# Performance work log

Hardware: AMD Instinct MI355X
Metric: run time of the kernel (lower is better)

Reference implementation:

```python
import jax, jax.numpy as jnp
import numpy as np
import math

# Model dims (see shape_source)
BATCH, SEQ, HH, WW = 32, 128, 32, 32   # x: (B, seq_len, H, W); L = H*W = 1024
D_MODEL = 1024                          # hidden_dim
N2 = 4                                  # n=8 -> 4 complex S4D modes
L_MAX = 64                              # SSM kernel length (l_max)


def _layernorm(x, gamma, beta, eps=1e-5):
    mu = jnp.mean(x, axis=-1, keepdims=True)
    var = jnp.var(x, axis=-1, keepdims=True)
    return (x - mu) * jax.lax.rsqrt(var + eps) * gamma + beta


def setup_inputs() -> dict:
    key = jax.random.key(0)
    ks = jax.random.split(key, 12)
    d_in = SEQ  # d_input = d_output = seq_len
    inp = {
        "x": jax.random.normal(ks[0], (BATCH, SEQ, HH, WW), dtype=jnp.float32),
        # encoder Linear(d_input -> d_model)
        "W_enc": jax.random.normal(ks[1], (d_in, D_MODEL), dtype=jnp.float32) / math.sqrt(d_in),
        "b_enc": jnp.zeros((D_MODEL,), dtype=jnp.float32),
        # S4D SSM parameters (per d_model channel, N2 complex modes)
        "log_dt": (jax.random.uniform(ks[2], (D_MODEL,), dtype=jnp.float32)
                   * (math.log(0.1) - math.log(0.001)) + math.log(0.001)),
        "A_log_real": jnp.full((D_MODEL, N2), math.log(0.5), dtype=jnp.float32),
        "A_imag": jnp.broadcast_to(math.pi * jnp.arange(N2, dtype=jnp.float32), (D_MODEL, N2)).copy(),
        "C_real": jax.random.normal(ks[3], (D_MODEL, N2), dtype=jnp.float32) * 0.5,
        "C_imag": jax.random.normal(ks[4], (D_MODEL, N2), dtype=jnp.float32) * 0.5,
        "D": jax.random.normal(ks[5], (D_MODEL,), dtype=jnp.float32),
        # position-wise GLU mixing Linear(d_model -> 2*d_model)
        "W_glu": jax.random.normal(ks[6], (D_MODEL, 2 * D_MODEL), dtype=jnp.float32) / math.sqrt(D_MODEL),
        "b_glu": jnp.zeros((2 * D_MODEL,), dtype=jnp.float32),
        "ln_gamma": jnp.ones((D_MODEL,), dtype=jnp.float32),
        "ln_beta": jnp.zeros((D_MODEL,), dtype=jnp.float32),
        # decoder Linear(d_model -> d_output)
        "W_dec": jax.random.normal(ks[7], (D_MODEL, d_in), dtype=jnp.float32) / math.sqrt(D_MODEL),
        "b_dec": jnp.zeros((d_in,), dtype=jnp.float32),
    }
    return inp


def reference(x, W_enc, b_enc, log_dt, A_log_real, A_imag, C_real, C_imag, D,
              W_glu, b_glu, ln_gamma, ln_beta, W_dec, b_dec):
    Bsz, S, Hh, Ww = x.shape
    L = Hh * Ww
    u = x.reshape(Bsz, S, L)                                  # (B, d_input, L)
    # encoder applied per position along L
    h = jnp.einsum('bdl,de->ble', u, W_enc) + b_enc           # (B, L, d_model)

    # ---- S4D kernel (ZOH discretization, B=1, diagonal A) ----
    dt = jnp.exp(log_dt)                                      # (d,)
    A = -jnp.exp(A_log_real) + 1j * A_imag                    # (d, n2) complex
    Cc = C_real + 1j * C_imag
    dtA = A * dt[:, None]                                     # (d, n2)
    Bd = (jnp.exp(dtA) - 1.0) / A                             # ZOH input matrix
    t = jnp.arange(L_MAX)
    vand = jnp.exp(dtA[:, :, None] * t)                       # (d, n2, l_max)
    K = 2.0 * jnp.einsum('dn,dnl->dl', Cc * Bd, vand).real    # (d, l_max)

    # ---- causal FFT convolution along L + skip D*u ----
    z = jnp.swapaxes(h, 1, 2)                                 # (B, d, L)
    n_fft = L + L_MAX
    y = jnp.fft.irfft(jnp.fft.rfft(z, n=n_fft) * jnp.fft.rfft(K, n=n_fft), n=n_fft)[..., :L]
    y = y + D[:, None] * z                                    # (B, d, L)

    # ---- block: GELU -> GLU mixing -> residual -> LayerNorm ----
    y = jax.nn.gelu(jnp.swapaxes(y, 1, 2))                    # (B, L, d)
    g = y @ W_glu + b_glu                                     # (B, L, 2d)
    g = g[..., :D_MODEL] * jax.nn.sigmoid(g[..., D_MODEL:])
    h = _layernorm(h + g, ln_gamma, ln_beta)                  # (B, L, d)

    out = h @ W_dec + b_dec                                   # (B, L, d_output)
    out = jnp.swapaxes(out, 1, 2).reshape(Bsz, S, Hh, Ww)
    return out
```

## Files before the change

### kernel.cpp

```cpp
#include <hip/hip_runtime.h>
#include <hip/hip_bf16.h>
#include <math.h>

#define B_ 32
#define S_ 128
#define L_ 1024
#define D_ 1024

typedef unsigned short u16;
typedef __attribute__((ext_vector_type(8))) __bf16 bf16x8;
typedef __attribute__((ext_vector_type(4))) float f32x4;

__device__ __forceinline__ float bf2f(u16 u) {
    return __uint_as_float(((unsigned)u) << 16);
}
__device__ __forceinline__ u16 f2bf(float f) {
    unsigned u = __float_as_uint(f);
    u += 0x7FFF + ((u >> 16) & 1);
    return (u16)(u >> 16);
}
__device__ __forceinline__ float gelu_tanh(float x) {
    float x3 = x * x * x;
    float t = tanhf(0.7978845608028654f * (x + 0.044715f * x3));
    return 0.5f * x * (1.0f + t);
}
__device__ __forceinline__ float sigmoidf(float x) {
    return 1.0f / (1.0f + expf(-x));
}
__device__ __forceinline__ void gld16(const void* g, void* l) {
    __builtin_amdgcn_global_load_lds((const __attribute__((address_space(1))) void*)g,
                                     (__attribute__((address_space(3))) void*)l, 16, 0, 0);
}

__global__ __launch_bounds__(256) void k_ssmk(
        const float* __restrict__ log_dt, const float* __restrict__ Alr,
        const float* __restrict__ Aim, const float* __restrict__ Cr,
        const float* __restrict__ Ci, float* __restrict__ Kt) {
    int tid = blockIdx.x * 256 + threadIdx.x;
    int d = tid & (D_ - 1);
    int j = tid >> 10;
    float dt = expf(log_dt[d]);
    float acc = 0.f;
    #pragma unroll
    for (int n = 0; n < 4; ++n) {
        float ar = -expf(Alr[d * 4 + n]);
        float ai = Aim[d * 4 + n];
        float wr = ar * dt, wi = ai * dt;
        float ew = expf(wr);
        float sw, cw; sincosf(wi, &sw, &cw);
        float ur = ew * cw - 1.0f, ui = ew * sw;
        float inv = 1.0f / (ar * ar + ai * ai);
        float bdr = (ur * ar + ui * ai) * inv;
        float bdi = (ui * ar - ur * ai) * inv;
        float cr = Cr[d * 4 + n], ci = Ci[d * 4 + n];
        float cbr = cr * bdr - ci * bdi;
        float cbi = cr * bdi + ci * bdr;
        float ej = expf(wr * (float)j);
        float sj, cj; sincosf(wi * (float)j, &sj, &cj);
        acc += 2.0f * ej * (cbr * cj - cbi * sj);
    }
    Kt[j * D_ + d] = acc;
}

__global__ __launch_bounds__(256) void k_zero(float* __restrict__ p) {
    int tid = blockIdx.x * 256 + threadIdx.x;
    *(float4*)&p[tid * 4] = make_float4(0.f, 0.f, 0.f, 0.f);
}

__global__ __launch_bounds__(256) void k_c12(
        const float* __restrict__ Wd, const float* __restrict__ gam,
        const float* __restrict__ bet, const float* __restrict__ bd,
        float* __restrict__ c12) {
    int s = blockIdx.x;
    int t = threadIdx.x;
    float a1 = 0.f, a2 = 0.f;
    #pragma unroll
    for (int it = 0; it < 4; ++it) {
        int k = it * 256 + t;
        float w = Wd[(size_t)k * 128 + s];
        a1 += gam[k] * w;
        a2 += bet[k] * w;
    }
    #pragma unroll
    for (int off = 32; off > 0; off >>= 1) {
        a1 += __shfl_down(a1, off);
        a2 += __shfl_down(a2, off);
    }
    __shared__ float r1[4], r2[4];
    int wid = t >> 6, lane = t & 63;
    if (lane == 0) { r1[wid] = a1; r2[wid] = a2; }
    __syncthreads();
    if (t == 0) {
        c12[s] = r1[0] + r1[1] + r1[2] + r1[3];
        c12[128 + s] = r2[0] + r2[1] + r2[2] + r2[3] + bd[s];
    }
}

__global__ __launch_bounds__(256) void k_tcast(
        const float* __restrict__ src0, u16* __restrict__ dst0, int R, int C,
        const float* __restrict__ rowscale) {
    __shared__ float tile[64][65];
    const float* src = src0 + (size_t)blockIdx.z * R * C;
    u16* dst = dst0 + (size_t)blockIdx.z * R * C;
    int c0 = blockIdx.x * 64;
    int r0 = blockIdx.y * 64;
    int t = threadIdx.x;
    #pragma unroll
    for (int p = 0; p < 4; ++p) {
        int fid = p * 256 + t;
        int rr = fid >> 4, cc = (fid & 15) * 4;
        float4 v = *(const float4*)&src[(size_t)(r0 + rr) * C + c0 + cc];
        float sc = rowscale ? rowscale[r0 + rr] : 1.0f;
        tile[rr][cc + 0] = v.x * sc; tile[rr][cc + 1] = v.y * sc;
        tile[rr][cc + 2] = v.z * sc; tile[rr][cc + 3] = v.w * sc;
    }
    __syncthreads();
    #pragma unroll
    for (int p = 0; p < 4; ++p) {
        int fid = p * 256 + t;
        int rr = fid >> 4, cc = (fid & 15) * 4;
        ushort4 o;
        o.x = f2bf(tile[cc + 0][rr]);
        o.y = f2bf(tile[cc + 1][rr]);
        o.z = f2bf(tile[cc + 2][rr]);
        o.w = f2bf(tile[cc + 3][rr]);
        *(ushort4*)&dst[(size_t)(c0 + rr) * R + r0 + cc] = o;
    }
}

__global__ __launch_bounds__(256) void k_enc_mfma(
        const u16* __restrict__ xb, const u16* __restrict__ WeT,
        const float* __restrict__ be, u16* __restrict__ hb) {
    __shared__ u16 As[128 * 128];
    __shared__ u16 Bs[128 * 128];
    int t = threadIdx.x;
    int lane = t & 63, wid = t >> 6;
    int wr = wid & 1, wc = wid >> 1;
    int orig = blockIdx.x;
    int wgid = (orig & 7) * 256 + (orig >> 3);
    int m0 = (wgid >> 3) * 128;
    int e0 = (wgid & 7) * 128;

    #pragma unroll
    for (int c = 0; c < 8; ++c) {
        int ch = wid * 8 + c;
        int r = ch * 4 + (lane >> 4);
        int g = (lane & 15) ^ (r & 15);
        gld16(&xb[(size_t)(m0 + r) * 128 + g * 8], &As[ch * 512]);
        gld16(&WeT[(size_t)(e0 + r) * 128 + g * 8], &Bs[ch * 512]);
    }
    int co4[4];
    #pragma unroll
    for (int kh = 0; kh < 4; ++kh)
        co4[kh] = ((((lane >> 4) + kh * 4) ^ (lane & 15)) * 8);
    int arow[4], brow[4];
    #pragma unroll
    for (int i = 0; i < 4; ++i) arow[i] = (wr * 64 + i * 16 + (lane & 15)) * 128;
    #pragma unroll
    for (int q = 0; q < 4; ++q) brow[q] = (wc * 64 + q * 16 + (lane & 15)) * 128;

    __syncthreads();
    f32x4 acc[4][4] = {};
    #pragma unroll
    for (int kh = 0; kh < 4; ++kh) {
        bf16x8 af[4], bfr[4];
        #pragma unroll
        for (int i = 0; i < 4; ++i) af[i] = *(const bf16x8*)&As[arow[i] + co4[kh]];
        #pragma unroll
        for (int q = 0; q < 4; ++q) bfr[q] = *(const bf16x8*)&Bs[brow[q] + co4[kh]];
        __builtin_amdgcn_s_setprio(1);
        #pragma unroll
        for (int i = 0; i < 4; ++i)
            #pragma unroll
            for (int q = 0; q < 4; ++q)
                acc[i][q] = __builtin_amdgcn_mfma_f32_16x16x32_bf16(af[i], bfr[q], acc[i][q], 0, 0, 0);
        __builtin_amdgcn_s_setprio(0);
    }
    #pragma unroll
    for (int q = 0; q < 4; ++q) {
        int e = e0 + wc * 64 + q * 16 + (lane & 15);
        float bias = be[e];
        #pragma unroll
        for (int i = 0; i < 4; ++i) {
            #pragma unroll
            for (int r = 0; r < 4; ++r) {
                int m = m0 + wr * 64 + i * 16 + (lane >> 4) * 4 + r;
                hb[(size_t)m * 1024 + e] = f2bf(acc[i][q][r] + bias);
            }
        }
    }
}

__global__ __launch_bounds__(256) void k_conv(
        const u16* __restrict__ hb, const float* __restrict__ Kt,
        const float* __restrict__ Dv, u16* __restrict__ yg) {
    __shared__ float hs[128][64];
    int b = blockIdx.z;
    int l0 = blockIdx.y * 64;
    int d0 = blockIdx.x * 64;
    int t = threadIdx.x;
    int dl = t & 63, lg = t >> 6;
    #pragma unroll
    for (int p = 0; p < 8; ++p) {
        int fid = p * 256 + t;
        int r = fid >> 4, c4 = fid & 15;
        int l = l0 - 64 + r;
        float4 v = make_float4(0.f, 0.f, 0.f, 0.f);
        if (l >= 0) {
            ushort4 u = *(const ushort4*)&hb[((size_t)b * 1024 + l) * 1024 + d0 + c4 * 4];
            v = make_float4(bf2f(u.x), bf2f(u.y), bf2f(u.z), bf2f(u.w));
        }
        *(float4*)&hs[r][c4 * 4] = v;
    }
    float kr[64];
    #pragma unroll
    for (int j = 0; j < 64; ++j) kr[j] = Kt[j * 1024 + d0 + dl];
    float Dd = Dv[d0 + dl];
    __syncthreads();
    float acc[16] = {};
    int rbase = lg * 16 + 1;
    #pragma unroll
    for (int s = 0; s < 15; ++s) {
        float hv = hs[rbase + s][dl];
        #pragma unroll
        for (int i = 0; i <= 14; ++i)
            if (i <= s) acc[i] = fmaf(kr[i + 63 - s], hv, acc[i]);
    }
    #pragma unroll
    for (int s = 15; s < 64; ++s) {
        float hv = hs[rbase + s][dl];
        #pragma unroll
        for (int i = 0; i < 16; ++i)
            acc[i] = fmaf(kr[i + 63 - s], hv, acc[i]);
    }
    #pragma unroll
    for (int s = 64; s < 79; ++s) {
        float hv = hs[rbase + s][dl];
        #pragma unroll
        for (int i = 1; i < 16; ++i)
            if (i >= s - 63) acc[i] = fmaf(kr[i + 63 - s], hv, acc[i]);
    }
    #pragma unroll
    for (int i = 0; i < 16; ++i) {
        int l = l0 + lg * 16 + i;
        float z = hs[64 + lg * 16 + i][dl];
        float y = acc[i] + Dd * z;
        yg[((size_t)b * 1024 + l) * 1024 + d0 + dl] = f2bf(gelu_tanh(y));
    }
}

__global__ __launch_bounds__(512, 2) void k_glu256(
        const u16* __restrict__ yg, const u16* __restrict__ WgT,
        const float* __restrict__ bg, u16* __restrict__ hb,
        float* __restrict__ rowS) {
    __shared__ __align__(16) u16 S[65536];
    int t = threadIdx.x;
    int lane = t & 63, wid = t >> 6;
    int wr = wid >> 2, wc = wid & 3;

    int orig = blockIdx.x;
    int wgid = (orig & 7) * 128 + (orig >> 3);
    int m0 = (wgid >> 3) * 256;
    int p0g = (wgid & 7) * 128;

    int gofs = (((lane & 7) ^ ((lane >> 3) & 7)) * 8);
    int ch0 = wid * 2, ch1 = ch0 + 1;
    int dst0 = ch0 * 512 + lane * 8;
    int dst1 = ch1 * 512 + lane * 8;
    int gmA[2][2], gmB[2][2];
    #pragma unroll
    for (int h = 0; h < 2; ++h) {
        #pragma unroll
        for (int j = 0; j < 2; ++j) {
            int ch = ch0 + j;
            gmA[h][j] = m0 + (ch >> 3) * 128 + h * 64 + (ch & 7) * 8 + (lane >> 3);
            int r = (ch >> 2) * 64 + h * 32 + (ch & 3) * 8 + (lane >> 3);
            gmB[h][j] = ((r >> 4) & 1) * 1024 + p0g + (((r >> 5) << 4) | (r & 15));
        }
    }
    int co[2];
    co[0] = (((lane >> 4) + 0) ^ (lane & 7)) * 8;
    co[1] = (((lane >> 4) + 4) ^ (lane & 7)) * 8;
    int arow[4], brow[2];
    #pragma unroll
    for (int i = 0; i < 4; ++i) arow[i] = (wr * 64 + i * 16 + (lane & 15)) * 64;
    #pragma unroll
    for (int q = 0; q < 2; ++q) brow[q] = (wc * 32 + q * 16 + (lane & 15)) * 64;

#define GLD_A(H, BUF, K0) { u16* d_ = &S[((BUF) * 2 + (H)) * 8192]; \
    gld16(&yg[(size_t)gmA[H][0] * 1024 + (K0) + gofs], d_ + dst0); \
    gld16(&yg[(size_t)gmA[H][1] * 1024 + (K0) + gofs], d_ + dst1); }
#define GLD_B(H, BUF, K0) { u16* d_ = &S[32768 + ((BUF) * 2 + (H)) * 8192]; \
    gld16(&WgT[(size_t)gmB[H][0] * 1024 + (K0) + gofs], d_ + dst0); \
    gld16(&WgT[(size_t)gmB[H][1] * 1024 + (K0) + gofs], d_ + dst1); }

#define RD_AH(MS) { const u16* Ar_ = &S[(cbuf * 2 + (MS)) * 8192]; \
    _Pragma("unroll") for (int i = 0; i < 4; ++i) { \
        a_[i][0] = *(const bf16x8*)&Ar_[arow[i] + co[0]]; \
        a_[i][1] = *(const bf16x8*)&Ar_[arow[i] + co[1]]; } }
#define RD_BH(NS, BB) { const u16* Br_ = &S[32768 + (cbuf * 2 + (NS)) * 8192]; \
    _Pragma("unroll") for (int q = 0; q < 2; ++q) { \
        BB[q][0] = *(const bf16x8*)&Br_[brow[q] + co[0]]; \
        BB[q][1] = *(const bf16x8*)&Br_[brow[q] + co[1]]; } }
#define MFMA16(MS, NS, BB) { __builtin_amdgcn_s_setprio(1); \
    _Pragma("unroll") for (int i = 0; i < 4; ++i) \
        _Pragma("unroll") for (int q = 0; q < 2; ++q) { \
            acc[(MS) * 4 + i][(NS) * 2 + q] = __builtin_amdgcn_mfma_f32_16x16x32_bf16( \
                a_[i][0], BB[q][0], acc[(MS) * 4 + i][(NS) * 2 + q], 0, 0, 0); \
            acc[(MS) * 4 + i][(NS) * 2 + q] = __builtin_amdgcn_mfma_f32_16x16x32_bf16( \
                a_[i][1], BB[q][1], acc[(MS) * 4 + i][(NS) * 2 + q], 0, 0, 0); } \
    __builtin_amdgcn_s_setprio(0); }
#define BAR() { __builtin_amdgcn_s_barrier(); __builtin_amdgcn_sched_barrier(0); }

    f32x4 acc[8][4] = {};
    bf16x8 a_[4][2], b0_[2][2], b1_[2][2];

    GLD_A(0, 0, 0); GLD_B(0, 0, 0); GLD_B(1, 0, 0); GLD_A(1, 0, 0);
    GLD_A(0, 1, 64); GLD_B(0, 1, 64);

    for (int kt = 0; kt < 15; ++kt) {
        int cbuf = kt & 1, nbuf = cbuf ^ 1;
        int k1 = (kt + 1) * 64, k2 = (kt + 2) * 64;
        asm volatile("s_waitcnt vmcnt(4)" ::: "memory");
        BAR();
        RD_BH(0, b0_); RD_BH(1, b1_); RD_AH(0);
        GLD_B(1, nbuf, k1);
        MFMA16(0, 0, b0_);
        BAR();
        GLD_A(1, nbuf, k1);
        MFMA16(0, 1, b1_);
        BAR();
        RD_AH(1);
        if (kt < 14) GLD_A(0, cbuf, k2);
        MFMA16(1, 0, b0_);
        BAR();
        if (kt < 14) GLD_B(0, cbuf, k2);
        MFMA16(1, 1, b1_);
    }
    {
        int cbuf = 1;
        asm volatile("s_waitcnt vmcnt(0)" ::: "memory");
        BAR();
        RD_BH(0, b0_); RD_BH(1, b1_); RD_AH(0);
        MFMA16(0, 0, b0_);
        MFMA16(0, 1, b1_);
        RD_AH(1);
        MFMA16(1, 0, b0_);
        MFMA16(1, 1, b1_);
    }
#undef GLD_A
#undef GLD_B
#undef RD_AH
#undef RD_BH
#undef MFMA16
#undef BAR

    float* Ts = (float*)S;
    int erow = t >> 3;
    int ecg = (t & 7) * 16;
    #pragma unroll
    for (int chunk = 0; chunk < 4; ++chunk) {
        __syncthreads();
        if (wr == (chunk >> 1)) {
            #pragma unroll
            for (int ii = 0; ii < 4; ++ii) {
                int i = (chunk & 1) * 4 + ii;
                #pragma unroll
                for (int pb = 0; pb < 2; ++pb) {
                    int col = (wc * 2 + pb) * 16 + (lane & 15);
                    float b1v = bg[p0g + col];
                    float b2v = bg[1024 + p0g + col];
                    #pragma unroll
                    for (int r = 0; r < 4; ++r) {
                        int rloc = ii * 16 + (lane >> 4) * 4 + r;
                        float g1 = acc[i][pb * 2][r] + b1v;
                        float g2 = acc[i][pb * 2 + 1][r] + b2v;
                        Ts[rloc * 132 + col] = g1 * sigmoidf(g2);
                    }
                }
            }
        }
        __syncthreads();
        int gm = m0 + chunk * 64 + erow;
        size_t gbase = (size_t)gm * 1024 + p0g + ecg;
        float rs1 = 0.f, rs2 = 0.f;
        #pragma unroll
        for (int h = 0; h < 2; ++h) {
            uint4 hv = *(uint4*)&hb[gbase + h * 8];
            u16* hu = (u16*)&hv;
            #pragma unroll
            for (int e = 0; e < 8; ++e) {
                float v = bf2f(hu[e]) + Ts[erow * 132 + ecg + h * 8 + e];
                rs1 += v;
                rs2 += v * v;
                hu[e] = f2bf(v);
            }
            *(uint4*)&hb[gbase + h * 8] = hv;
        }
        rs1 += __shfl_xor(rs1, 1); rs2 += __shfl_xor(rs2, 1);
        rs1 += __shfl_xor(rs1, 2); rs2 += __shfl_xor(rs2, 2);
        rs1 += __shfl_xor(rs1, 4); rs2 += __shfl_xor(rs2, 4);
        if ((lane & 7) == 0) {
            atomicAdd(&rowS[gm], rs1);
            atomicAdd(&rowS[32768 + gm], rs2);
        }
    }
}

__global__ __launch_bounds__(256) void k_dec_mfma(
        const u16* __restrict__ hb, const u16* __restrict__ WdT,
        const float* __restrict__ rowS, const float* __restrict__ c12,
        float* __restrict__ out) {
    __shared__ __align__(16) char smem[66560];
    u16* As = (u16*)smem;
    u16* Bs = (u16*)(smem + 32768);
    float* Ts = (float*)smem;
    float* muL = (float*)(smem + 65536);
    float* rsL = (float*)(smem + 65536 + 512);
    int t = threadIdx.x;
    int lane = t & 63, wid = t >> 6;
    int wr = wid & 1, wc = wid >> 1;
    int m0 = blockIdx.x * 128;
    int bb = m0 >> 10, l0 = m0 & 1023;

    if (t < 128) {
        float s1 = rowS[m0 + t];
        float s2 = rowS[32768 + m0 + t];
        float mu = s1 * (1.0f / 1024.0f);
        float var = s2 * (1.0f / 1024.0f) - mu * mu;
        muL[t] = mu;
        rsL[t] = rsqrtf(var + 1e-5f);
    }

    int gsrc = (((lane & 7) ^ (lane >> 3)) * 8);
    int rr4[4];
    #pragma unroll
    for (int c = 0; c < 4; ++c) rr4[c] = (wid * 4 + c) * 8 + (lane >> 3);
    int co[2];
    co[0] = (((lane >> 4) + 0) ^ (lane & 7)) * 8;
    co[1] = (((lane >> 4) + 4) ^ (lane & 7)) * 8;
    int arow[4], brow[4];
    #pragma unroll
    for (int i = 0; i < 4; ++i) arow[i] = (wr * 64 + i * 16 + (lane & 15)) * 64;
    #pragma unroll
    for (int q = 0; q < 4; ++q) brow[q] = (wc * 64 + q * 16 + (lane & 15)) * 64;

    f32x4 acc[4][4] = {};
    #pragma unroll
    for (int c = 0; c < 4; ++c) {
        int ch = wid * 4 + c;
        gld16(&hb[(size_t)(m0 + rr4[c]) * 1024 + gsrc], &As[0 * 8192 + ch * 512]);
        gld16(&WdT[(size_t)rr4[c] * 1024 + gsrc], &Bs[0 * 8192 + ch * 512]);
    }
    __syncthreads();
    int cur = 0;
    for (int kt = 0; kt < 16; ++kt) {
        if (kt < 15) {
            int k0 = (kt + 1) * 64;
            #pragma unroll
            for (int c = 0; c < 4; ++c) {
                int ch = wid * 4 + c;
                gld16(&hb[(size_t)(m0 + rr4[c]) * 1024 + k0 + gsrc], &As[(cur ^ 1) * 8192 + ch * 512]);
                gld16(&WdT[(size_t)rr4[c] * 1024 + k0 + gsrc], &Bs[(cur ^ 1) * 8192 + ch * 512]);
            }
        }
        #pragma unroll
        for (int kh = 0; kh < 2; ++kh) {
            bf16x8 af[4], bfr[4];
            #pragma unroll
            for (int i = 0; i < 4; ++i) af[i] = *(const bf16x8*)&As[cur * 8192 + arow[i] + co[kh]];
            #pragma unroll
            for (int q = 0; q < 4; ++q) bfr[q] = *(const bf16x8*)&Bs[cur * 8192 + brow[q] + co[kh]];
            __builtin_amdgcn_s_setprio(1);
            #pragma unroll
            for (int i = 0; i < 4; ++i)
                #pragma unroll
                for (int q = 0; q < 4; ++q)
                    acc[i][q] = __builtin_amdgcn_mfma_f32_16x16x32_bf16(af[i], bfr[q], acc[i][q], 0, 0, 0);
            __builtin_amdgcn_s_setprio(0);
        }
        __syncthreads();
        cur ^= 1;
    }
    __syncthreads();
    #pragma unroll
    for (int ro = 0; ro < 2; ++ro) {
        if (wc == ro) {
            #pragma unroll
            for (int i = 0; i < 4; ++i)
                #pragma unroll
                for (int q = 0; q < 4; ++q) {
                    int sl = q * 16 + (lane & 15);
                    float c1v = c12[ro * 64 + sl];
                    float c2v = c12[128 + ro * 64 + sl];
                    #pragma unroll
                    for (int r = 0; r < 4; ++r) {
                        int ml = wr * 64 + i * 16 + (lane >> 4) * 4 + r;
                        float rst = rsL[ml];
                        Ts[sl * 132 + ml] = rst * acc[i][q][r] - muL[ml] * rst * c1v + c2v;
                    }
                }
        }
        __syncthreads();
        #pragma unroll
        for (int p = 0; p < 8; ++p) {
            int fid = p * 256 + t;
            int sl = fid >> 5, c = (fid & 31) * 4;
            float4 v = *(const float4*)&Ts[sl * 132 + c];
            *(float4*)&out[(size_t)bb * 131072 + (size_t)(ro * 64 + sl) * 1024 + l0 + c] = v;
        }
        __syncthreads();
    }
}

extern "C" void kernel_launch(void* const* d_in, const int* in_sizes, int n_in,
                              void* d_out, int out_size, void* d_ws, size_t ws_size,
                              hipStream_t stream) {
    (void)in_sizes; (void)n_in; (void)out_size; (void)ws_size;
    const float* x   = (const float*)d_in[0];
    const float* We  = (const float*)d_in[1];
    const float* be  = (const float*)d_in[2];
    const float* ldt = (const float*)d_in[3];
    const float* Alr = (const float*)d_in[4];
    const float* Aim = (const float*)d_in[5];
    const float* Cr  = (const float*)d_in[6];
    const float* Ci  = (const float*)d_in[7];
    const float* Dv  = (const float*)d_in[8];
    const float* Wg  = (const float*)d_in[9];
    const float* bg  = (const float*)d_in[10];
    const float* gam = (const float*)d_in[11];
    const float* bet = (const float*)d_in[12];
    const float* Wd  = (const float*)d_in[13];
    const float* bd  = (const float*)d_in[14];
    float* out = (float*)d_out;

    u16* hb = (u16*)d_ws;
    u16* yg = hb + 33554432ull;
    float* Kt = (float*)(yg + 33554432ull);
    u16* WgT = (u16*)(Kt + 65536);
    u16* WdT = WgT + 2097152ull;
    u16* WeT = WdT + 131072ull;
    u16* xb  = yg;
    float* rowS = Kt;
    float* c12  = (float*)WeT;

    k_tcast<<<dim3(32, 16, 1), 256, 0, stream>>>(Wg, WgT, 1024, 2048, nullptr);
    k_tcast<<<dim3(2, 16, 1), 256, 0, stream>>>(Wd, WdT, 1024, 128, gam);
    k_tcast<<<dim3(16, 2, 1), 256, 0, stream>>>(We, WeT, 128, 1024, nullptr);
    k_tcast<<<dim3(16, 2, 32), 256, 0, stream>>>(x, xb, 128, 1024, nullptr);
    k_ssmk<<<256, 256, 0, stream>>>(ldt, Alr, Aim, Cr, Ci, Kt);
    k_enc_mfma<<<2048, 256, 0, stream>>>(xb, WeT, be, hb);
    k_conv<<<dim3(16, 16, 32), 256, 0, stream>>>(hb, Kt, Dv, yg);
    k_c12<<<128, 256, 0, stream>>>(Wd, gam, bet, bd, c12);
    k_zero<<<64, 256, 0, stream>>>(rowS);
    k_glu256<<<1024, 512, 0, stream>>>(yg, WgT, bg, hb, rowS);
    k_dec_mfma<<<256, 256, 0, stream>>>(hb, WdT, rowS, c12, out);
}
```

Measured before the change: 336.2 us.

## Move LayerNorm row statistics into decoder GEMM and stream conv over sequence

```diff
diff --git a/kernel.cpp b/kernel.cpp
--- a/kernel.cpp
+++ b/kernel.cpp
@@ -9,6 +9,7 @@
 
 typedef unsigned short u16;
 typedef __attribute__((ext_vector_type(8))) __bf16 bf16x8;
+typedef __attribute__((ext_vector_type(8))) short short8;
 typedef __attribute__((ext_vector_type(4))) float f32x4;
 
 __device__ __forceinline__ float bf2f(u16 u) {
@@ -62,11 +63,6 @@
     Kt[j * D_ + d] = acc;
 }
 
-__global__ __launch_bounds__(256) void k_zero(float* __restrict__ p) {
-    int tid = blockIdx.x * 256 + threadIdx.x;
-    *(float4*)&p[tid * 4] = make_float4(0.f, 0.f, 0.f, 0.f);
-}
-
 __global__ __launch_bounds__(256) void k_c12(
         const float* __restrict__ Wd, const float* __restrict__ gam,
         const float* __restrict__ bet, const float* __restrict__ bd,
@@ -194,66 +190,77 @@
 __global__ __launch_bounds__(256) void k_conv(
         const u16* __restrict__ hb, const float* __restrict__ Kt,
         const float* __restrict__ Dv, u16* __restrict__ yg) {
-    __shared__ float hs[128][64];
-    int b = blockIdx.z;
-    int l0 = blockIdx.y * 64;
+    __shared__ float hs[128][68];
+    int b = blockIdx.y;
     int d0 = blockIdx.x * 64;
     int t = threadIdx.x;
     int dl = t & 63, lg = t >> 6;
-    #pragma unroll
-    for (int p = 0; p < 8; ++p) {
-        int fid = p * 256 + t;
-        int r = fid >> 4, c4 = fid & 15;
-        int l = l0 - 64 + r;
-        float4 v = make_float4(0.f, 0.f, 0.f, 0.f);
-        if (l >= 0) {
-            ushort4 u = *(const ushort4*)&hb[((size_t)b * 1024 + l) * 1024 + d0 + c4 * 4];
-            v = make_float4(bf2f(u.x), bf2f(u.y), bf2f(u.z), bf2f(u.w));
-        }
-        *(float4*)&hs[r][c4 * 4] = v;
+    {
+        int r = 64 + (t >> 2), cg0 = (t & 3) * 16;
+        #pragma unroll
+        for (int j = 0; j < 4; ++j)
+            *(float4*)&hs[r][cg0 + j * 4] = make_float4(0.f, 0.f, 0.f, 0.f);
     }
     float kr[64];
     #pragma unroll
     for (int j = 0; j < 64; ++j) kr[j] = Kt[j * 1024 + d0 + dl];
     float Dd = Dv[d0 + dl];
-    __syncthreads();
-    float acc[16] = {};
-    int rbase = lg * 16 + 1;
-    #pragma unroll
-    for (int s = 0; s < 15; ++s) {
-        float hv = hs[rbase + s][dl];
-        #pragma unroll
-        for (int i = 0; i <= 14; ++i)
-            if (i <= s) acc[i] = fmaf(kr[i + 63 - s], hv, acc[i]);
-    }
-    #pragma unroll
-    for (int s = 15; s < 64; ++s) {
-        float hv = hs[rbase + s][dl];
-        #pragma unroll
-        for (int i = 0; i < 16; ++i)
-            acc[i] = fmaf(kr[i + 63 - s], hv, acc[i]);
-    }
-    #pragma unroll
-    for (int s = 64; s < 79; ++s) {
-        float hv = hs[rbase + s][dl];
-        #pragma unroll
-        for (int i = 1; i < 16; ++i)
-            if (i >= s - 63) acc[i] = fmaf(kr[i + 63 - s], hv, acc[i]);
-    }
-    #pragma unroll
-    for (int i = 0; i < 16; ++i) {
-        int l = l0 + lg * 16 + i;
-        float z = hs[64 + lg * 16 + i][dl];
-        float y = acc[i] + Dd * z;
-        yg[((size_t)b * 1024 + l) * 1024 + d0 + dl] = f2bf(gelu_tanh(y));
+    int lr = t >> 2, cg = (t & 3) * 16;
+    for (int it = 0; it < 16; ++it) {
+        int l0 = it * 64;
+        {
+            int l = l0 + lr;
+            int row = l & 127;
+            const u16* src = &hb[((size_t)b * 1024 + l) * 1024 + d0 + cg];
+            #pragma unroll
+            for (int h = 0; h < 2; ++h) {
+                ushort4 u0 = *(const ushort4*)&src[h * 8];
+                ushort4 u1 = *(const ushort4*)&src[h * 8 + 4];
+                *(float4*)&hs[row][cg + h * 8] =
+                    make_float4(bf2f(u0.x), bf2f(u0.y), bf2f(u0.z), bf2f(u0.w));
+                *(float4*)&hs[row][cg + h * 8 + 4] =
+                    make_float4(bf2f(u1.x), bf2f(u1.y), bf2f(u1.z), bf2f(u1.w));
+            }
+        }
+        __syncthreads();
+        float acc[16] = {};
+        int rb = l0 + 65 + lg * 16;
+        #pragma unroll
+        for (int s = 0; s < 15; ++s) {
+            float hv = hs[(rb + s) & 127][dl];
+            #pragma unroll
+            for (int i = 0; i <= 14; ++i)
+                if (i <= s) acc[i] = fmaf(kr[i + 63 - s], hv, acc[i]);
+        }
+        #pragma unroll
+        for (int s = 15; s < 64; ++s) {
+            float hv = hs[(rb + s) & 127][dl];
+            #pragma unroll
+            for (int i = 0; i < 16; ++i)
+                acc[i] = fmaf(kr[i + 63 - s], hv, acc[i]);
+        }
+        #pragma unroll
+        for (int s = 64; s < 79; ++s) {
+            float hv = hs[(rb + s) & 127][dl];
+            #pragma unroll
+            for (int i = 1; i < 16; ++i)
+                if (i >= s - 63) acc[i] = fmaf(kr[i + 63 - s], hv, acc[i]);
+        }
+        #pragma unroll
+        for (int i = 0; i < 16; ++i) {
+            int l = l0 + lg * 16 + i;
+            float z = hs[l & 127][dl];
+            float y = acc[i] + Dd * z;
+            yg[((size_t)b * 1024 + l) * 1024 + d0 + dl] = f2bf(gelu_tanh(y));
+        }
+        __syncthreads();
     }
 }
 
 __global__ __launch_bounds__(512, 2) void k_glu256(
         const u16* __restrict__ yg, const u16* __restrict__ WgT,
-        const float* __restrict__ bg, u16* __restrict__ hb,
-        float* __restrict__ rowS) {
-    __shared__ __align__(16) u16 S[65536];
+        const float* __restrict__ bg, u16* __restrict__ hb) {
+    __shared__ u16 S[65536];
     int t = threadIdx.x;
     int lane = t & 63, wid = t >> 6;
     int wr = wid >> 2, wc = wid & 3;
@@ -355,62 +362,28 @@
 #undef MFMA16
 #undef BAR
 
-    float* Ts = (float*)S;
-    int erow = t >> 3;
-    int ecg = (t & 7) * 16;
-    #pragma unroll
-    for (int chunk = 0; chunk < 4; ++chunk) {
-        __syncthreads();
-        if (wr == (chunk >> 1)) {
-            #pragma unroll
-            for (int ii = 0; ii < 4; ++ii) {
-                int i = (chunk & 1) * 4 + ii;
-                #pragma unroll
-                for (int pb = 0; pb < 2; ++pb) {
-                    int col = (wc * 2 + pb) * 16 + (lane & 15);
-                    float b1v = bg[p0g + col];
-                    float b2v = bg[1024 + p0g + col];
-                    #pragma unroll
-                    for (int r = 0; r < 4; ++r) {
-                        int rloc = ii * 16 + (lane >> 4) * 4 + r;
-                        float g1 = acc[i][pb * 2][r] + b1v;
-                        float g2 = acc[i][pb * 2 + 1][r] + b2v;
-                        Ts[rloc * 132 + col] = g1 * sigmoidf(g2);
-                    }
-                }
+    #pragma unroll
+    for (int i = 0; i < 8; ++i) {
+        #pragma unroll
+        for (int pb = 0; pb < 2; ++pb) {
+            int col = p0g + (wc * 2 + pb) * 16 + (lane & 15);
+            float b1v = bg[col];
+            float b2v = bg[1024 + col];
+            #pragma unroll
+            for (int r = 0; r < 4; ++r) {
+                int m = m0 + wr * 128 + i * 16 + (lane >> 4) * 4 + r;
+                size_t idx = (size_t)m * 1024 + col;
+                float g1 = acc[i][pb * 2][r] + b1v;
+                float g2 = acc[i][pb * 2 + 1][r] + b2v;
+                hb[idx] = f2bf(bf2f(hb[idx]) + g1 * sigmoidf(g2));
             }
-        }
-        __syncthreads();
-        int gm = m0 + chunk * 64 + erow;
-        size_t gbase = (size_t)gm * 1024 + p0g + ecg;
-        float rs1 = 0.f, rs2 = 0.f;
-        #pragma unroll
-        for (int h = 0; h < 2; ++h) {
-            uint4 hv = *(uint4*)&hb[gbase + h * 8];
-            u16* hu = (u16*)&hv;
-            #pragma unroll
-            for (int e = 0; e < 8; ++e) {
-                float v = bf2f(hu[e]) + Ts[erow * 132 + ecg + h * 8 + e];
-                rs1 += v;
-                rs2 += v * v;
-                hu[e] = f2bf(v);
-            }
-            *(uint4*)&hb[gbase + h * 8] = hv;
-        }
-        rs1 += __shfl_xor(rs1, 1); rs2 += __shfl_xor(rs2, 1);
-        rs1 += __shfl_xor(rs1, 2); rs2 += __shfl_xor(rs2, 2);
-        rs1 += __shfl_xor(rs1, 4); rs2 += __shfl_xor(rs2, 4);
-        if ((lane & 7) == 0) {
-            atomicAdd(&rowS[gm], rs1);
-            atomicAdd(&rowS[32768 + gm], rs2);
         }
     }
 }
 
 __global__ __launch_bounds__(256) void k_dec_mfma(
         const u16* __restrict__ hb, const u16* __restrict__ WdT,
-        const float* __restrict__ rowS, const float* __restrict__ c12,
-        float* __restrict__ out) {
+        const float* __restrict__ c12, float* __restrict__ out) {
     __shared__ __align__(16) char smem[66560];
     u16* As = (u16*)smem;
     u16* Bs = (u16*)(smem + 32768);
@@ -423,15 +396,6 @@
     int m0 = blockIdx.x * 128;
     int bb = m0 >> 10, l0 = m0 & 1023;
 
-    if (t < 128) {
-        float s1 = rowS[m0 + t];
-        float s2 = rowS[32768 + m0 + t];
-        float mu = s1 * (1.0f / 1024.0f);
-        float var = s2 * (1.0f / 1024.0f) - mu * mu;
-        muL[t] = mu;
-        rsL[t] = rsqrtf(var + 1e-5f);
-    }
-
     int gsrc = (((lane & 7) ^ (lane >> 3)) * 8);
     int rr4[4];
     #pragma unroll
@@ -446,6 +410,7 @@
     for (int q = 0; q < 4; ++q) brow[q] = (wc * 64 + q * 16 + (lane & 15)) * 64;
 
     f32x4 acc[4][4] = {};
+    float s1[4] = {}, s2[4] = {};
     #pragma unroll
     for (int c = 0; c < 4; ++c) {
         int ch = wid * 4 + c;
@@ -471,6 +436,18 @@
             for (int i = 0; i < 4; ++i) af[i] = *(const bf16x8*)&As[cur * 8192 + arow[i] + co[kh]];
             #pragma unroll
             for (int q = 0; q < 4; ++q) bfr[q] = *(const bf16x8*)&Bs[cur * 8192 + brow[q] + co[kh]];
+            if (wid < 2) {
+                #pragma unroll
+                for (int i = 0; i < 4; ++i) {
+                    short8 sa = *(short8*)&af[i];
+                    #pragma unroll
+                    for (int e = 0; e < 8; ++e) {
+                        float v = bf2f((u16)sa[e]);
+                        s1[i] += v;
+                        s2[i] = fmaf(v, v, s2[i]);
+                    }
+                }
+            }
             __builtin_amdgcn_s_setprio(1);
             #pragma unroll
             for (int i = 0; i < 4; ++i)
@@ -481,6 +458,22 @@
         }
         __syncthreads();
         cur ^= 1;
+    }
+    if (wid < 2) {
+        #pragma unroll
+        for (int i = 0; i < 4; ++i) {
+            s1[i] += __shfl_xor(s1[i], 16);
+            s2[i] += __shfl_xor(s2[i], 16);
+            s1[i] += __shfl_xor(s1[i], 32);
+            s2[i] += __shfl_xor(s2[i], 32);
+            if (lane < 16) {
+                int ml = wr * 64 + i * 16 + lane;
+                float mu = s1[i] * (1.0f / 1024.0f);
+                float var = s2[i] * (1.0f / 1024.0f) - mu * mu;
+                muL[ml] = mu;
+                rsL[ml] = rsqrtf(var + 1e-5f);
+            }
+        }
     }
     __syncthreads();
     #pragma unroll
@@ -541,7 +534,6 @@
     u16* WdT = WgT + 2097152ull;
     u16* WeT = WdT + 131072ull;
     u16* xb  = yg;
-    float* rowS = Kt;
     float* c12  = (float*)WeT;
 
     k_tcast<<<dim3(32, 16, 1), 256, 0, stream>>>(Wg, WgT, 1024, 2048, nullptr);
@@ -550,9 +542,8 @@
     k_tcast<<<dim3(16, 2, 32), 256, 0, stream>>>(x, xb, 128, 1024, nullptr);
     k_ssmk<<<256, 256, 0, stream>>>(ldt, Alr, Aim, Cr, Ci, Kt);
     k_enc_mfma<<<2048, 256, 0, stream>>>(xb, WeT, be, hb);
-    k_conv<<<dim3(16, 16, 32), 256, 0, stream>>>(hb, Kt, Dv, yg);
+    k_conv<<<dim3(16, 32), 256, 0, stream>>>(hb, Kt, Dv, yg);
     k_c12<<<128, 256, 0, stream>>>(Wd, gam, bet, bd, c12);
-    k_zero<<<64, 256, 0, stream>>>(rowS);
-    k_glu256<<<1024, 512, 0, stream>>>(yg, WgT, bg, hb, rowS);
-    k_dec_mfma<<<256, 256, 0, stream>>>(hb, WdT, rowS, c12, out);
-}
+    k_glu256<<<1024, 512, 0, stream>>>(yg, WgT, bg, hb);
+    k_dec_mfma<<<256, 256, 0, stream>>>(hb, WdT, c12, out);
+}
```

After: 328.4 us. 2.3% less time.
